# Optimization experiments

Measured on AMD Instinct MI355X. Metric: run time of the kernel, lower is better.

## Reference

```python
import jax, jax.numpy as jnp
import numpy as np

B, A, T = 256, 512, 21
DIM = 128
SC = 6
NHEAD, HD = 4, DIM // 4

def conv1d_relu(x, w, b, stride=2):
    # x: (N, C, L), w: (O, I, K)
    y = jax.lax.conv_general_dilated(x, w, (stride,), 'SAME', dimension_numbers=('NCH', 'OIH', 'NCH'))
    return jax.nn.relu(y + b[None, :, None])

def to_vector(feat, vm):
    vec_mask = vm[..., :-1] & vm[..., 1:]
    while vec_mask.ndim < feat.ndim:
        vec_mask = vec_mask[..., None]
    return jnp.where(vec_mask, feat[:, :, 1:] - feat[:, :, :-1], jnp.zeros_like(feat[:, :, 1:]))

def setup_inputs():
    key = jax.random.key(0)
    ks = jax.random.split(key, 24)
    f32 = jnp.float32
    inp = {}
    inp['position'] = jax.random.normal(ks[0], (B, A, T, 2), f32)
    inp['heading'] = jax.random.normal(ks[1], (B, A, T), f32)
    inp['velocity'] = jax.random.normal(ks[2], (B, A, T, 2), f32)
    inp['shape'] = jax.random.uniform(ks[3], (B, A, T, 2), f32)
    inp['current_state'] = jax.random.normal(ks[4], (B, SC), f32)
    inp['category'] = jax.random.randint(ks[5], (B, A), 0, 4)
    inp['valid_mask'] = jax.random.randint(ks[6], (B, A, T), 0, 2).astype(bool)
    # history encoder (CNN) params: 9 -> 32 -> 64 -> 128 channels, k=3, stride 2
    inp['conv1_w'] = jax.random.normal(ks[7], (32, 9, 3), f32) * 0.1
    inp['conv1_b'] = jnp.zeros((32,), f32)
    inp['conv2_w'] = jax.random.normal(ks[8], (64, 32, 3), f32) * 0.1
    inp['conv2_b'] = jnp.zeros((64,), f32)
    inp['conv3_w'] = jax.random.normal(ks[9], (128, 64, 3), f32) * 0.1
    inp['conv3_b'] = jnp.zeros((128,), f32)
    # StateAttentionEncoder params
    inp['se_w'] = jax.random.normal(ks[10], (SC, DIM), f32) * 0.02   # per-channel Linear(1,dim) weights
    inp['se_b'] = jnp.zeros((SC, DIM), f32)
    inp['pos_embed'] = jax.random.normal(ks[11], (1, SC, DIM), f32) * 0.02
    inp['query'] = jax.random.normal(ks[12], (1, 1, DIM), f32) * 0.02
    inp['in_proj_w'] = jax.random.normal(ks[13], (3 * DIM, DIM), f32) * (1.0 / np.sqrt(DIM))
    inp['in_proj_b'] = jnp.zeros((3 * DIM,), f32)
    inp['out_proj_w'] = jax.random.normal(ks[14], (DIM, DIM), f32) * (1.0 / np.sqrt(DIM))
    inp['out_proj_b'] = jnp.zeros((DIM,), f32)
    inp['type_emb'] = jax.random.normal(ks[15], (4, DIM), f32) * 0.02
    return inp

def reference(position, heading, velocity, shape, current_state, category, valid_mask,
              conv1_w, conv1_b, conv2_w, conv2_b, conv3_w, conv3_b,
              se_w, se_b, pos_embed, query, in_proj_w, in_proj_b, out_proj_w, out_proj_b,
              type_emb):
    # --- build per-step agent features (B, A, T-1, 9) ---
    heading_vec = to_vector(heading, valid_mask)
    valid_mask_vec = valid_mask[..., 1:] & valid_mask[..., :-1]
    agent_feature = jnp.concatenate([
        to_vector(position, valid_mask),
        to_vector(velocity, valid_mask),
        jnp.stack([jnp.cos(heading_vec), jnp.sin(heading_vec)], axis=-1),
        shape[:, :, 1:],
        valid_mask_vec.astype(jnp.float32)[..., None],
    ], axis=-1)
    bs, nA, Tm1, C = agent_feature.shape
    x = agent_feature.reshape(bs * nA, Tm1, C).transpose(0, 2, 1)  # (N, 9, T-1)
    # --- history CNN encoder (applied to all rows, then masked; same math as boolean gather/scatter) ---
    h = conv1d_relu(x, conv1_w, conv1_b)
    h = conv1d_relu(h, conv2_w, conv2_b)
    h = conv1d_relu(h, conv3_w, conv3_b)
    enc = h.mean(axis=-1)  # (N, DIM)
    valid_agent = valid_mask.any(-1).reshape(-1)
    x_agent = jnp.where(valid_agent[:, None], enc, 0.0).reshape(bs, nA, DIM)
    # --- ego state attention encoder (eval mode: no token dropout) ---
    ego = current_state[:, :SC]
    x_embed = ego[:, :, None] * se_w[None] + se_b[None] + pos_embed  # (B, SC, DIM)
    Wq, Wk, Wv = in_proj_w[:DIM], in_proj_w[DIM:2 * DIM], in_proj_w[2 * DIM:]
    bq, bk, bv = in_proj_b[:DIM], in_proj_b[DIM:2 * DIM], in_proj_b[2 * DIM:]
    q = (query[0, 0] @ Wq.T + bq).reshape(NHEAD, HD)             # (H, D)
    k = (x_embed @ Wk.T + bk).reshape(bs, SC, NHEAD, HD)          # (B, S, H, D)
    v = (x_embed @ Wv.T + bv).reshape(bs, SC, NHEAD, HD)
    scores = jnp.einsum('hd,bshd->bhs', q, k) * (1.0 / np.sqrt(HD))
    attn = jax.nn.softmax(scores, axis=-1)
    o = jnp.einsum('bhs,bshd->bhd', attn, v).reshape(bs, DIM)
    x_ego = o @ out_proj_w.T + out_proj_b                         # (B, DIM)
    x_agent = x_agent.at[:, 0].set(x_ego)
    # --- type embedding add ---
    return x_agent + type_emb[category]
```

## Files before the change

### kernel.cpp

```cpp
#include <hip/hip_runtime.h>
#include <hip/hip_bf16.h>


#define BB 256
#define AAG 512
#define TT 21
#define NAG (BB * AAG)
#define AB 12
#define NB1 ((NAG + AB - 1) / AB)

typedef __hip_bfloat16 bf16;
typedef __attribute__((ext_vector_type(8))) short s8v;
typedef __attribute__((ext_vector_type(4))) float f4v;

__device__ int g_dtype;
__device__ int g_mask_mode;
__device__ __align__(16) short g_w1p[32 * 64];
__device__ __align__(16) short g_w2p[64 * 96];
__device__ __align__(16) short g_w3p[128 * 192];
__device__ __align__(16) float g_b1[32];
__device__ __align__(16) float g_b2[64];
__device__ __align__(16) float g_b3[128];
__device__ __align__(16) float g_wqk[4 * 128];
__device__ __align__(16) float g_qb[4];

template <int DT>
__device__ __forceinline__ float ldf(const void* p, long i) {
    if (DT) return __bfloat162float(((const bf16*)p)[i]);
    return ((const float*)p)[i];
}
template <int DT>
__device__ __forceinline__ void stf(void* p, long i, float v) {
    if (DT) ((bf16*)p)[i] = __float2bfloat16(v);
    else    ((float*)p)[i] = v;
}
__device__ __forceinline__ unsigned short f2bu(float x) {
    bf16 b = __float2bfloat16(x);
    union { bf16 b; unsigned short u; } cv; cv.b = b; return cv.u;
}
__device__ __forceinline__ float bu2f(unsigned short u) {
    union { unsigned int i; float f; } cv; cv.i = ((unsigned int)u) << 16; return cv.f;
}
template <int DT>
__device__ __forceinline__ float2 ldf2(const void* p, long i) {
    if (DT) {
        unsigned int u = *(const unsigned int*)((const bf16*)p + i);
        return make_float2(bu2f((unsigned short)(u & 0xffffu)),
                           bu2f((unsigned short)(u >> 16)));
    }
    return *(const float2*)((const float*)p + i);
}
__device__ __forceinline__ bool mask_at(const void* p, long i, int mode) {
    if (mode == 0) return ((const int*)p)[i] != 0;
    if (mode == 1) return ((const unsigned char*)p)[i] != 0;
    if (mode == 2) return ((const float*)p)[i] != 0.f;
    return (((const unsigned short*)p)[i] & 0x7fff) != 0;
}

template <int DT>
__device__ __forceinline__ float rowdot64(const void* W, long off, const float* y) {
    float acc = 0.f;
    if (DT) {
        const unsigned short* wr = (const unsigned short*)W + off;
#pragma unroll
        for (int i = 0; i < 8; i++) {
            uint4 w = *(const uint4*)(wr + i * 8);
            acc = fmaf(bu2f((unsigned short)(w.x & 0xffffu)), y[i * 8 + 0], acc);
            acc = fmaf(bu2f((unsigned short)(w.x >> 16)),     y[i * 8 + 1], acc);
            acc = fmaf(bu2f((unsigned short)(w.y & 0xffffu)), y[i * 8 + 2], acc);
            acc = fmaf(bu2f((unsigned short)(w.y >> 16)),     y[i * 8 + 3], acc);
            acc = fmaf(bu2f((unsigned short)(w.z & 0xffffu)), y[i * 8 + 4], acc);
            acc = fmaf(bu2f((unsigned short)(w.z >> 16)),     y[i * 8 + 5], acc);
            acc = fmaf(bu2f((unsigned short)(w.w & 0xffffu)), y[i * 8 + 6], acc);
            acc = fmaf(bu2f((unsigned short)(w.w >> 16)),     y[i * 8 + 7], acc);
        }
    } else {
        const float* wr = (const float*)W + off;
#pragma unroll
        for (int i = 0; i < 16; i++) {
            float4 w = *(const float4*)(wr + i * 4);
            acc = fmaf(w.x, y[i * 4 + 0], acc);
            acc = fmaf(w.y, y[i * 4 + 1], acc);
            acc = fmaf(w.z, y[i * 4 + 2], acc);
            acc = fmaf(w.w, y[i * 4 + 3], acc);
        }
    }
    return acc;
}

template <int DT>
__device__ __forceinline__ void prep_body(const void* w1, const void* b1,
                                          const void* w2, const void* b2,
                                          const void* w3, const void* b3) {
    int tid = blockIdx.x * 256 + threadIdx.x;
    const int nt = 64 * 256;
    for (int i = tid; i < 32 * 64; i += nt) {
        int oc = i >> 6, k = i & 63, tap = k >> 4, ic = k & 15;
        float v = (tap < 3 && ic < 9) ? ldf<DT>(w1, oc * 27 + ic * 3 + tap) : 0.f;
        g_w1p[i] = (short)f2bu(v);
    }
    for (int i = tid; i < 64 * 96; i += nt) {
        int oc = i / 96, k = i % 96, tap = k >> 5, ic = k & 31;
        g_w2p[i] = (short)f2bu(ldf<DT>(w2, oc * 96 + ic * 3 + tap));
    }
    for (int i = tid; i < 128 * 192; i += nt) {
        int oc = i / 192, k = i % 192, tap = k >> 6, ic = k & 63;
        g_w3p[i] = (short)f2bu(ldf<DT>(w3, oc * 192 + ic * 3 + tap));
    }
    for (int i = tid; i < 32; i += nt) g_b1[i] = ldf<DT>(b1, i);
    for (int i = tid; i < 64; i += nt) g_b2[i] = ldf<DT>(b2, i);
    for (int i = tid; i < 128; i += nt) g_b3[i] = ldf<DT>(b3, i);
}

template <int DT>
__device__ __forceinline__ void qprep_body(const void* query, const void* ipw,
                                           const void* ipb, float* sq) {
    int tid = threadIdx.x;
    if (tid < 128) {
        float acc = ldf<DT>(ipb, tid);
        for (int e = 0; e < 128; e++)
            acc = fmaf(ldf<DT>(query, e), ldf<DT>(ipw, (long)tid * 128 + e), acc);
        sq[tid] = acc;
    }
    __syncthreads();
    int e = tid & 127, hb = tid >> 7;
    for (int h = hb; h < 4; h += 2) {
        float acc = 0.f;
#pragma unroll
        for (int j = 0; j < 32; j++)
            acc = fmaf(sq[h * 32 + j], ldf<DT>(ipw, (long)(128 + h * 32 + j) * 128 + e), acc);
        g_wqk[h * 128 + e] = acc;
    }
    if (tid < 4) {
        float acc = 0.f;
#pragma unroll
        for (int j = 0; j < 32; j++)
            acc = fmaf(sq[tid * 32 + j], ldf<DT>(ipb, 128 + tid * 32 + j), acc);
        g_qb[tid] = acc;
    }
}

__global__ __launch_bounds__(256) void prep_kernel(
    const unsigned int* __restrict__ pw, const unsigned char* __restrict__ m,
    const void* __restrict__ w1, const void* __restrict__ b1,
    const void* __restrict__ w2, const void* __restrict__ b2,
    const void* __restrict__ w3, const void* __restrict__ b3,
    const void* __restrict__ query, const void* __restrict__ ipw,
    const void* __restrict__ ipb) {
    __shared__ int cls[4];
    __shared__ int mv;
    __shared__ int good;
    __shared__ float sq[128];
    int tid = threadIdx.x;
    if (tid < 4) cls[tid] = 0;
    if (tid == 0) { mv = 0; good = 0; }
    __syncthreads();
    int g = 0;
    for (int i = tid; i < 1024; i += 256) {
        unsigned int w = pw[i];
        unsigned int h0 = w & 0xffffu, h1 = w >> 16;
        unsigned int e0 = (h0 >> 7) & 0xff, e1 = (h1 >> 7) & 0xff;
        if (h0 == 0 || (e0 >= 90 && e0 <= 160)) g++;
        if (h1 == 0 || (e1 >= 90 && e1 <= 160)) g++;
    }
    atomicAdd(&good, g);
    int l0 = 0, l1 = 0, l2 = 0, l3 = 0, lm = 0;
    for (int i = tid; i < 4096; i += 256) {
        int v = m[i];
        if (v) {
            switch (i & 3) { case 0: l0 = 1; break; case 1: l1 = 1; break;
                             case 2: l2 = 1; break; default: l3 = 1; }
            if (v > lm) lm = v;
        }
    }
    if (l0) atomicOr(&cls[0], 1);
    if (l1) atomicOr(&cls[1], 1);
    if (l2) atomicOr(&cls[2], 1);
    if (l3) atomicOr(&cls[3], 1);
    atomicMax(&mv, lm);
    __syncthreads();
    int dt = (good >= 1740) ? 1 : 0;
    int mode;
    if (!cls[1] && !cls[2] && !cls[3]) mode = 0;
    else if (!cls[0] && !cls[1])       mode = 2;
    else if (mv <= 1)                  mode = 1;
    else                               mode = 3;
    if (blockIdx.x == 0 && tid == 0) { g_dtype = dt; g_mask_mode = mode; }

    if (blockIdx.x < 64) {
        if (dt) prep_body<1>(w1, b1, w2, b2, w3, b3);
        else    prep_body<0>(w1, b1, w2, b2, w3, b3);
    } else {
        if (dt) qprep_body<1>(query, ipw, ipb, sq);
        else    qprep_body<0>(query, ipw, ipb, sq);
    }
}

#define FEAT_RS 24
#define FEAT_AS 568
#define H1_RS 40
#define H1_AS 440
#define H2_RS 72
#define H2_AS 504
#define C3_AS 392
#define OFF_H1 6816
#define OFF_VALID 24192
#define SMEM_BYTES 24240

#define MFMA16(a, b, c) __builtin_amdgcn_mfma_f32_16x16x32_bf16((a), (b), (c), 0, 0, 0)

template <int DT>
__device__ __forceinline__ void stage1_body(
    const void* pos, const void* heading, const void* vel, const void* shp,
    const void* vmask, const int* category, const void* type_emb, void* out,
    char* smem, long agent0) {
    short* feat = (short*)smem;
    short* h1   = (short*)smem + OFF_H1;
    short* h2   = (short*)smem;
    short* c3   = (short*)smem + OFF_H1;
    int* s_valid = (int*)(smem + OFF_VALID);

    const int tid = threadIdx.x;
    const int wave = tid >> 6, lane = tid & 63;
    const int col = lane & 15, quad = lane >> 4;
    const int cg = col < AB ? col : AB - 1;
    const int mode = g_mask_mode;

    if (tid < AB * 16) {
        unsigned int* h1u = (unsigned int*)h1;
        h1u[(tid >> 4) * 220 + 200 + (tid & 15)] = 0;
    }
    for (int idx = tid; idx < AB * 22; idx += 256) {
        int ag = idx / 22, t = idx % 22;
        long agl = agent0 + ag;
        bool live = agl < NAG;
        short* row = feat + ag * FEAT_AS + t * FEAT_RS;
        if (t == 0) {
            int v = 0;
            if (live) {
                long b0 = agl * TT;
#pragma unroll
                for (int tt = 0; tt < TT; tt++)
                    v |= mask_at(vmask, b0 + tt, mode) ? 1 : 0;
            }
            s_valid[ag] = v;
        }
        if (t >= 20 || !live) {
            *(uint4*)row = make_uint4(0, 0, 0, 0);
            *(uint4*)(row + 8) = make_uint4(0, 0, 0, 0);
        } else {
            long base = agl * TT + t;
            bool vmt = mask_at(vmask, base, mode);
            bool m2 = vmt && mask_at(vmask, base + 1, mode);
            float2 pa = ldf2<DT>(pos, base * 2), pb = ldf2<DT>(pos, base * 2 + 2);
            float2 va = ldf2<DT>(vel, base * 2), vb = ldf2<DT>(vel, base * 2 + 2);
            float hh0 = ldf<DT>(heading, base), hh1 = ldf<DT>(heading, base + 1);
            float2 sv = ldf2<DT>(shp, base * 2 + 2);
            float dh = m2 ? (hh1 - hh0) : 0.f;
            float sn, cn;
            __sincosf(dh, &sn, &cn);
            unsigned int p0 = f2bu(m2 ? pb.x - pa.x : 0.f) | ((unsigned int)f2bu(m2 ? pb.y - pa.y : 0.f) << 16);
            unsigned int p1 = f2bu(m2 ? vb.x - va.x : 0.f) | ((unsigned int)f2bu(m2 ? vb.y - va.y : 0.f) << 16);
            unsigned int p2 = f2bu(cn) | ((unsigned int)f2bu(sn) << 16);
            unsigned int p3 = f2bu(sv.x) | ((unsigned int)f2bu(sv.y) << 16);
            unsigned int p4 = (unsigned int)f2bu(m2 ? 1.f : 0.f);
            *(uint4*)row = make_uint4(p0, p1, p2, p3);
            *(uint4*)(row + 8) = make_uint4(p4, 0, 0, 0);
        }
    }
    __syncthreads();

    {
        int Mt = wave >> 1;
        int oc = Mt * 16 + col;
        s8v a0 = *(const s8v*)(g_w1p + oc * 64 + quad * 8);
        s8v a1 = *(const s8v*)(g_w1p + oc * 64 + 32 + quad * 8);
        int k0 = quad * 8, k1 = 32 + quad * 8;
        int tap0 = k0 >> 4, ic0 = k0 & 15;
        int tap1 = k1 >> 4, ic1 = k1 & 15;
        int ocr = Mt * 16 + quad * 4;
        f4v bia = *(const f4v*)(g_b1 + ocr);
        const short* agbase = feat + cg * FEAT_AS;
#pragma unroll
        for (int i = 0; i < 5; i++) {
            int p = (wave & 1) * 5 + i;
            const short* bb = agbase + 2 * p * FEAT_RS;
            s8v b0 = *(const s8v*)(bb + tap0 * FEAT_RS + ic0);
            s8v b1 = *(const s8v*)(bb + tap1 * FEAT_RS + ic1);
            f4v acc = {0.f, 0.f, 0.f, 0.f};
            acc = MFMA16(a0, b0, acc);
            acc = MFMA16(a1, b1, acc);
            if (col < AB) {
                unsigned int lo = f2bu(fmaxf(acc[0] + bia[0], 0.f)) | ((unsigned int)f2bu(fmaxf(acc[1] + bia[1], 0.f)) << 16);
                unsigned int hi = f2bu(fmaxf(acc[2] + bia[2], 0.f)) | ((unsigned int)f2bu(fmaxf(acc[3] + bia[3], 0.f)) << 16);
                *(uint2*)(h1 + col * H1_AS + p * H1_RS + ocr) = make_uint2(lo, hi);
            }
        }
    }
    __syncthreads();

    {
        unsigned int* h2u = (unsigned int*)h2;
        for (int i = tid; i < AB * 64; i += 256) {
            int a2 = i >> 6, r = (i >> 5) & 1, cc = i & 31;
            h2u[a2 * 252 + r * 216 + cc] = 0;
        }
        int Mt = wave;
        int oc = Mt * 16 + col;
        s8v a[3];
#pragma unroll
        for (int ks = 0; ks < 3; ks++)
            a[ks] = *(const s8v*)(g_w2p + oc * 96 + ks * 32 + quad * 8);
        int ocr = Mt * 16 + quad * 4;
        f4v bia = *(const f4v*)(g_b2 + ocr);
#pragma unroll
        for (int p = 0; p < 5; p++) {
            f4v acc = {0.f, 0.f, 0.f, 0.f};
#pragma unroll
            for (int ks = 0; ks < 3; ks++) {
                s8v b = *(const s8v*)(h1 + cg * H1_AS + (2 * p + ks) * H1_RS + quad * 8);
                acc = MFMA16(a[ks], b, acc);
            }
            if (col < AB) {
                unsigned int lo = f2bu(fmaxf(acc[0] + bia[0], 0.f)) | ((unsigned int)f2bu(fmaxf(acc[1] + bia[1], 0.f)) << 16);
                unsigned int hi = f2bu(fmaxf(acc[2] + bia[2], 0.f)) | ((unsigned int)f2bu(fmaxf(acc[3] + bia[3], 0.f)) << 16);
                *(uint2*)(h2 + col * H2_AS + (p + 1) * H2_RS + ocr) = make_uint2(lo, hi);
            }
        }
    }
    __syncthreads();

#pragma unroll
    for (int m2 = 0; m2 < 2; m2++) {
        int Mt = wave * 2 + m2;
        int oc = Mt * 16 + col;
        s8v a[6];
#pragma unroll
        for (int ks = 0; ks < 6; ks++)
            a[ks] = *(const s8v*)(g_w3p + oc * 192 + ks * 32 + quad * 8);
        int ocr = Mt * 16 + quad * 4;
        f4v bia = *(const f4v*)(g_b3 + ocr);
#pragma unroll
        for (int p = 0; p < 3; p++) {
            f4v acc = {0.f, 0.f, 0.f, 0.f};
#pragma unroll
            for (int ks = 0; ks < 6; ks++) {
                int kg = ks * 32 + quad * 8;
                int tap = kg >> 6, ic = kg & 63;
                s8v b = *(const s8v*)(h2 + cg * H2_AS + (2 * p + tap) * H2_RS + ic);
                acc = MFMA16(a[ks], b, acc);
            }
            if (col < AB) {
                unsigned int lo = f2bu(fmaxf(acc[0] + bia[0], 0.f)) | ((unsigned int)f2bu(fmaxf(acc[1] + bia[1], 0.f)) << 16);
                unsigned int hi = f2bu(fmaxf(acc[2] + bia[2], 0.f)) | ((unsigned int)f2bu(fmaxf(acc[3] + bia[3], 0.f)) << 16);
                *(uint2*)(c3 + col * C3_AS + p * 128 + ocr) = make_uint2(lo, hi);
            }
        }
    }
    __syncthreads();

    if (tid < AB * 16) {
        int ag = tid >> 4;
        int ocg = (tid & 15) * 8;
        long agl = agent0 + ag;
        if (agl < NAG) {
            const short* cb = c3 + ag * C3_AS;
            s8v x0 = *(const s8v*)(cb + ocg);
            s8v x1 = *(const s8v*)(cb + 128 + ocg);
            s8v x2 = *(const s8v*)(cb + 256 + ocg);
            int valid = s_valid[ag];
            int cat = category[agl];
            float vals[8];
#pragma unroll
            for (int j = 0; j < 8; j++) {
                float m = (bu2f((unsigned short)x0[j]) + bu2f((unsigned short)x1[j]) +
                           bu2f((unsigned short)x2[j])) * (1.f / 3.f);
                vals[j] = valid ? m : 0.f;
            }
            if (DT) {
                s8v te = *(const s8v*)((const bf16*)type_emb + (long)cat * 128 + ocg);
                s8v o;
#pragma unroll
                for (int j = 0; j < 8; j++)
                    o[j] = (short)f2bu(vals[j] + bu2f((unsigned short)te[j]));
                *(s8v*)((bf16*)out + agl * 128 + ocg) = o;
            } else {
                const float4* tep = (const float4*)((const float*)type_emb + (long)cat * 128 + ocg);
                float4 t0 = tep[0], t1 = tep[1];
                float4 o0 = make_float4(vals[0] + t0.x, vals[1] + t0.y, vals[2] + t0.z, vals[3] + t0.w);
                float4 o1 = make_float4(vals[4] + t1.x, vals[5] + t1.y, vals[6] + t1.z, vals[7] + t1.w);
                float4* op = (float4*)((float*)out + agl * 128 + ocg);
                op[0] = o0; op[1] = o1;
            }
        }
    }
}

__global__ __launch_bounds__(256) void stage1_kernel(
    const void* __restrict__ pos, const void* __restrict__ heading,
    const void* __restrict__ vel, const void* __restrict__ shp,
    const void* __restrict__ vmask, const int* __restrict__ category,
    const void* __restrict__ type_emb, void* __restrict__ out) {
    __shared__ __align__(16) char smem[SMEM_BYTES];
    long agent0 = (long)blockIdx.x * AB;
    if (g_dtype) stage1_body<1>(pos, heading, vel, shp, vmask, category, type_emb, out, smem, agent0);
    else         stage1_body<0>(pos, heading, vel, shp, vmask, category, type_emb, out, smem, agent0);
}

template <int DT>
__device__ __forceinline__ void stage2_body(
    const void* cs, const int* category,
    const void* se_w, const void* se_b, const void* pe,
    const void* ipw, const void* ipb, const void* opw, const void* opb,
    const void* type_emb, void* out, float* sm) {
    const int b = blockIdx.x;
    const int tid = threadIdx.x;
    const int d = tid & 127, half = tid >> 7;

    float* s_xe  = sm;
    float* s_y   = s_xe + 768;
    float* s_sc  = s_y + 512;
    float* s_att = s_sc + 32;
    float* s_o   = s_att + 32;
    float* s_par = s_o + 128;

    for (int idx = tid; idx < 768; idx += 256) {
        int s = idx >> 7, dd = idx & 127;
        float ego = ldf<DT>(cs, b * 6 + s);
        s_xe[idx] = fmaf(ego, ldf<DT>(se_w, s * 128 + dd),
                         ldf<DT>(se_b, s * 128 + dd) + ldf<DT>(pe, s * 128 + dd));
    }
    __syncthreads();

    if (tid < 96) {
        int g = tid >> 2, lig = tid & 3;
        int h = g / 6, s = g - h * 6;
        const float* xr = s_xe + s * 128 + lig * 32;
        const float* wr = g_wqk + h * 128 + lig * 32;
        float t = 0.f;
#pragma unroll
        for (int e = 0; e < 32; e++) t = fmaf(xr[e], wr[e], t);
        t += __shfl_xor(t, 1, 4);
        t += __shfl_xor(t, 2, 4);
        if (lig == 0) s_sc[g] = (t + g_qb[h]) * 0.17677669529663687f;
    }
    __syncthreads();

    if (tid < 4) {
        float mx = -1e30f;
#pragma unroll
        for (int s = 0; s < 6; s++) mx = fmaxf(mx, s_sc[tid * 6 + s]);
        float sum = 0.f, ex[6];
#pragma unroll
        for (int s = 0; s < 6; s++) { ex[s] = expf(s_sc[tid * 6 + s] - mx); sum += ex[s]; }
        float inv = 1.f / sum;
#pragma unroll
        for (int s = 0; s < 6; s++) s_att[tid * 6 + s] = ex[s] * inv;
    }
    __syncthreads();

    for (int idx = tid; idx < 512; idx += 256) {
        int h = idx >> 7, e = idx & 127;
        float y = 0.f;
#pragma unroll
        for (int s = 0; s < 6; s++) y = fmaf(s_att[h * 6 + s], s_xe[s * 128 + e], y);
        s_y[idx] = y;
    }
    __syncthreads();

    {
        int h = d >> 5;
        const float* yr = s_y + h * 128 + half * 64;
        s_par[half * 128 + d] = rowdot64<DT>(ipw, (long)(256 + d) * 128 + half * 64, yr);
    }
    __syncthreads();
    if (half == 0) s_o[d] = s_par[d] + s_par[128 + d] + ldf<DT>(ipb, 256 + d);
    __syncthreads();

    {
        const float* orr = s_o + half * 64;
        s_par[half * 128 + d] = rowdot64<DT>(opw, (long)d * 128 + half * 64, orr);
    }
    __syncthreads();
    if (half == 0) {
        float x = s_par[d] + s_par[128 + d] + ldf<DT>(opb, d);
        int cat = category[(long)b * AAG];
        stf<DT>(out, (long)b * AAG * 128 + d, x + ldf<DT>(type_emb, cat * 128 + d));
    }
}

__global__ __launch_bounds__(256) void stage2_kernel(
    const void* __restrict__ cs, const int* __restrict__ category,
    const void* __restrict__ se_w, const void* __restrict__ se_b,
    const void* __restrict__ pe,
    const void* __restrict__ ipw, const void* __restrict__ ipb,
    const void* __restrict__ opw, const void* __restrict__ opb,
    const void* __restrict__ type_emb, void* __restrict__ out) {
    __shared__ float sm[1728];
    if (g_dtype) stage2_body<1>(cs, category, se_w, se_b, pe, ipw, ipb, opw, opb, type_emb, out, sm);
    else         stage2_body<0>(cs, category, se_w, se_b, pe, ipw, ipb, opw, opb, type_emb, out, sm);
}

extern "C" void kernel_launch(void* const* d_in, const int* in_sizes, int n_in,
                              void* d_out, int out_size, void* d_ws, size_t ws_size,
                              hipStream_t stream) {
    const void* position      = d_in[0];
    const void* heading       = d_in[1];
    const void* velocity      = d_in[2];
    const void* shape         = d_in[3];
    const void* current_state = d_in[4];
    const int*  category      = (const int*)d_in[5];
    const void* valid_mask    = d_in[6];
    const void* conv1_w = d_in[7];
    const void* conv1_b = d_in[8];
    const void* conv2_w = d_in[9];
    const void* conv2_b = d_in[10];
    const void* conv3_w = d_in[11];
    const void* conv3_b = d_in[12];
    const void* se_w    = d_in[13];
    const void* se_b    = d_in[14];
    const void* pos_embed = d_in[15];
    const void* query     = d_in[16];
    const void* in_proj_w = d_in[17];
    const void* in_proj_b = d_in[18];
    const void* out_proj_w = d_in[19];
    const void* out_proj_b = d_in[20];
    const void* type_emb   = d_in[21];

    hipLaunchKernelGGL(prep_kernel, dim3(65), dim3(256), 0, stream,
                       (const unsigned int*)position, (const unsigned char*)valid_mask,
                       conv1_w, conv1_b, conv2_w, conv2_b, conv3_w, conv3_b,
                       query, in_proj_w, in_proj_b);

    hipLaunchKernelGGL(stage1_kernel, dim3(NB1), dim3(256), 0, stream,
                       position, heading, velocity, shape, valid_mask, category,
                       type_emb, d_out);

    hipLaunchKernelGGL(stage2_kernel, dim3(BB), dim3(256), 0, stream,
                       current_state, category, se_w, se_b, pos_embed,
                       in_proj_w, in_proj_b, out_proj_w, out_proj_b, type_emb, d_out);
}
```

Before: 331.9 us.

## Process four 16-agent chunks per block with register prefetch of next chunk

The stage1 kernel now handles 16 agents per MFMA tile instead of 12, so all 16 columns of each 16x16 MFMA are used. Each block loops over four chunks and prefetches the next chunk's raw inputs into registers while the current chunk runs its convolutions. The per-agent valid flag is now accumulated with atomicOr from the per-timestep mask loads rather than a separate 21-step scan, and syncthreads is replaced by an explicit lgkmcnt wait plus barrier. This cuts grid size and redundant mask reads. In exchange it raises register pressure from the prefetched values and uses more LDS per block.

```diff
diff --git a/kernel.cpp b/kernel.cpp
--- a/kernel.cpp
+++ b/kernel.cpp
@@ -6,8 +6,9 @@
 #define AAG 512
 #define TT 21
 #define NAG (BB * AAG)
-#define AB 12
-#define NB1 ((NAG + AB - 1) / AB)
+#define AB 16
+#define CHUNKS 4
+#define GRID1 (NAG / (AB * CHUNKS))
 
 typedef __hip_bfloat16 bf16;
 typedef __attribute__((ext_vector_type(8))) short s8v;
@@ -41,20 +42,48 @@
 __device__ __forceinline__ float bu2f(unsigned short u) {
     union { unsigned int i; float f; } cv; cv.i = ((unsigned int)u) << 16; return cv.f;
 }
-template <int DT>
-__device__ __forceinline__ float2 ldf2(const void* p, long i) {
-    if (DT) {
-        unsigned int u = *(const unsigned int*)((const bf16*)p + i);
-        return make_float2(bu2f((unsigned short)(u & 0xffffu)),
-                           bu2f((unsigned short)(u >> 16)));
-    }
-    return *(const float2*)((const float*)p + i);
-}
 __device__ __forceinline__ bool mask_at(const void* p, long i, int mode) {
     if (mode == 0) return ((const int*)p)[i] != 0;
     if (mode == 1) return ((const unsigned char*)p)[i] != 0;
     if (mode == 2) return ((const float*)p)[i] != 0.f;
     return (((const unsigned short*)p)[i] & 0x7fff) != 0;
+}
+
+template <int DT> struct RawV { using T2 = float2; using T1 = float; };
+template <> struct RawV<1> { using T2 = unsigned int; using T1 = unsigned short; };
+
+__device__ __forceinline__ float2 dec2v(float2 v) { return v; }
+__device__ __forceinline__ float2 dec2v(unsigned int u) {
+    return make_float2(bu2f((unsigned short)(u & 0xffffu)), bu2f((unsigned short)(u >> 16)));
+}
+__device__ __forceinline__ float dec1v(float v) { return v; }
+__device__ __forceinline__ float dec1v(unsigned short u) { return bu2f(u); }
+
+template <int DT>
+__device__ __forceinline__ typename RawV<DT>::T2 ldr2(const void* p, long i) {
+    if constexpr (DT) return *(const unsigned int*)((const bf16*)p + i);
+    else return *(const float2*)((const float*)p + i);
+}
+template <int DT>
+__device__ __forceinline__ typename RawV<DT>::T1 ldr1(const void* p, long i) {
+    if constexpr (DT) return ((const unsigned short*)p)[i];
+    else return ((const float*)p)[i];
+}
+__device__ __forceinline__ unsigned int mask_raw(const void* p, long i, int mode) {
+    if (mode == 0) return ((const unsigned int*)p)[i];
+    if (mode == 1) return ((const unsigned char*)p)[i];
+    if (mode == 2) return ((const unsigned int*)p)[i];
+    return ((const unsigned short*)p)[i];
+}
+__device__ __forceinline__ bool mask_dec(unsigned int r, int mode) {
+    if (mode == 2) return (r & 0x7fffffffu) != 0;
+    if (mode == 3) return (r & 0x7fffu) != 0;
+    return r != 0;
+}
+
+__device__ __forceinline__ void bar_lds() {
+    asm volatile("s_waitcnt lgkmcnt(0)" ::: "memory");
+    __builtin_amdgcn_s_barrier();
 }
 
 template <int DT>
@@ -203,17 +232,44 @@
 #define H2_RS 72
 #define H2_AS 504
 #define C3_AS 392
-#define OFF_H1 6816
-#define OFF_VALID 24192
-#define SMEM_BYTES 24240
+#define OFF_H1 9088
+#define OFF_VALID 32256
+#define SMEM_BYTES 32384
 
 #define MFMA16(a, b, c) __builtin_amdgcn_mfma_f32_16x16x32_bf16((a), (b), (c), 0, 0, 0)
+
+template <int DT>
+__device__ __forceinline__ void emit_row(
+    short* feat, int* vcur, int ag, int t, int mode,
+    unsigned int m0r, unsigned int m1r,
+    typename RawV<DT>::T2 par, typename RawV<DT>::T2 pbr,
+    typename RawV<DT>::T2 var, typename RawV<DT>::T2 vbr,
+    typename RawV<DT>::T1 h0r, typename RawV<DT>::T1 h1r,
+    typename RawV<DT>::T2 svr) {
+    bool vmt = mask_dec(m0r, mode);
+    bool m2 = vmt && mask_dec(m1r, mode);
+    if (vmt) atomicOr(&vcur[ag], 1);
+    float2 pa = dec2v(par), pb = dec2v(pbr), va = dec2v(var), vb = dec2v(vbr);
+    float hh0 = dec1v(h0r), hh1 = dec1v(h1r);
+    float2 sv = dec2v(svr);
+    float dh = m2 ? (hh1 - hh0) : 0.f;
+    float sn, cn;
+    __sincosf(dh, &sn, &cn);
+    unsigned int p0 = f2bu(m2 ? pb.x - pa.x : 0.f) | ((unsigned int)f2bu(m2 ? pb.y - pa.y : 0.f) << 16);
+    unsigned int p1 = f2bu(m2 ? vb.x - va.x : 0.f) | ((unsigned int)f2bu(m2 ? vb.y - va.y : 0.f) << 16);
+    unsigned int p2 = f2bu(cn) | ((unsigned int)f2bu(sn) << 16);
+    unsigned int p3 = f2bu(sv.x) | ((unsigned int)f2bu(sv.y) << 16);
+    unsigned int p4 = (unsigned int)f2bu(m2 ? 1.f : 0.f);
+    short* row = feat + ag * FEAT_AS + t * FEAT_RS;
+    *(uint4*)row = make_uint4(p0, p1, p2, p3);
+    *(uint4*)(row + 8) = make_uint4(p4, 0, 0, 0);
+}
 
 template <int DT>
 __device__ __forceinline__ void stage1_body(
     const void* pos, const void* heading, const void* vel, const void* shp,
     const void* vmask, const int* category, const void* type_emb, void* out,
-    char* smem, long agent0) {
+    char* smem) {
     short* feat = (short*)smem;
     short* h1   = (short*)smem + OFF_H1;
     short* h2   = (short*)smem;
@@ -223,152 +279,163 @@
     const int tid = threadIdx.x;
     const int wave = tid >> 6, lane = tid & 63;
     const int col = lane & 15, quad = lane >> 4;
-    const int cg = col < AB ? col : AB - 1;
     const int mode = g_mask_mode;
-
-    if (tid < AB * 16) {
-        unsigned int* h1u = (unsigned int*)h1;
-        h1u[(tid >> 4) * 220 + 200 + (tid & 15)] = 0;
-    }
-    for (int idx = tid; idx < AB * 22; idx += 256) {
-        int ag = idx / 22, t = idx % 22;
-        long agl = agent0 + ag;
-        bool live = agl < NAG;
-        short* row = feat + ag * FEAT_AS + t * FEAT_RS;
-        if (t == 0) {
-            int v = 0;
-            if (live) {
-                long b0 = agl * TT;
-#pragma unroll
-                for (int tt = 0; tt < TT; tt++)
-                    v |= mask_at(vmask, b0 + tt, mode) ? 1 : 0;
-            }
-            s_valid[ag] = v;
-        }
-        if (t >= 20 || !live) {
-            *(uint4*)row = make_uint4(0, 0, 0, 0);
-            *(uint4*)(row + 8) = make_uint4(0, 0, 0, 0);
-        } else {
-            long base = agl * TT + t;
-            bool vmt = mask_at(vmask, base, mode);
-            bool m2 = vmt && mask_at(vmask, base + 1, mode);
-            float2 pa = ldf2<DT>(pos, base * 2), pb = ldf2<DT>(pos, base * 2 + 2);
-            float2 va = ldf2<DT>(vel, base * 2), vb = ldf2<DT>(vel, base * 2 + 2);
-            float hh0 = ldf<DT>(heading, base), hh1 = ldf<DT>(heading, base + 1);
-            float2 sv = ldf2<DT>(shp, base * 2 + 2);
-            float dh = m2 ? (hh1 - hh0) : 0.f;
-            float sn, cn;
-            __sincosf(dh, &sn, &cn);
-            unsigned int p0 = f2bu(m2 ? pb.x - pa.x : 0.f) | ((unsigned int)f2bu(m2 ? pb.y - pa.y : 0.f) << 16);
-            unsigned int p1 = f2bu(m2 ? vb.x - va.x : 0.f) | ((unsigned int)f2bu(m2 ? vb.y - va.y : 0.f) << 16);
-            unsigned int p2 = f2bu(cn) | ((unsigned int)f2bu(sn) << 16);
-            unsigned int p3 = f2bu(sv.x) | ((unsigned int)f2bu(sv.y) << 16);
-            unsigned int p4 = (unsigned int)f2bu(m2 ? 1.f : 0.f);
-            *(uint4*)row = make_uint4(p0, p1, p2, p3);
-            *(uint4*)(row + 8) = make_uint4(p4, 0, 0, 0);
-        }
-    }
-    __syncthreads();
-
-    {
-        int Mt = wave >> 1;
-        int oc = Mt * 16 + col;
-        s8v a0 = *(const s8v*)(g_w1p + oc * 64 + quad * 8);
-        s8v a1 = *(const s8v*)(g_w1p + oc * 64 + 32 + quad * 8);
-        int k0 = quad * 8, k1 = 32 + quad * 8;
-        int tap0 = k0 >> 4, ic0 = k0 & 15;
-        int tap1 = k1 >> 4, ic1 = k1 & 15;
-        int ocr = Mt * 16 + quad * 4;
-        f4v bia = *(const f4v*)(g_b1 + ocr);
-        const short* agbase = feat + cg * FEAT_AS;
-#pragma unroll
-        for (int i = 0; i < 5; i++) {
-            int p = (wave & 1) * 5 + i;
-            const short* bb = agbase + 2 * p * FEAT_RS;
-            s8v b0 = *(const s8v*)(bb + tap0 * FEAT_RS + ic0);
-            s8v b1 = *(const s8v*)(bb + tap1 * FEAT_RS + ic1);
-            f4v acc = {0.f, 0.f, 0.f, 0.f};
-            acc = MFMA16(a0, b0, acc);
-            acc = MFMA16(a1, b1, acc);
-            if (col < AB) {
+    const long agent0_blk = (long)blockIdx.x * (AB * CHUNKS);
+
+    const int ag1 = tid / 20, t1 = tid % 20;
+    const int ag2 = (256 + tid) / 20, t2 = (256 + tid) % 20;
+    const bool zrow = (tid >= 96 && tid < 128);
+    const int zi = tid - 96, zag = zi >> 1;
+    const bool zth = zrow && !(zi & 1);
+
+    typename RawV<DT>::T2 pa1{}, pb1{}, va1{}, vb1{}, pa2{}, pb2{}, va2{}, vb2{};
+    typename RawV<DT>::T1 h01{}, h11{};
+    unsigned int m01 = 0, m11 = 0, m02 = 0, m12 = 0, mz = 0;
+
+    auto prefetch = [&](int c) {
+        long a0c = agent0_blk + (long)c * AB;
+        {
+            long base = (a0c + ag1) * TT + t1;
+            m01 = mask_raw(vmask, base, mode);
+            m11 = mask_raw(vmask, base + 1, mode);
+            pa1 = ldr2<DT>(pos, base * 2); pb1 = ldr2<DT>(pos, base * 2 + 2);
+            va1 = ldr2<DT>(vel, base * 2); vb1 = ldr2<DT>(vel, base * 2 + 2);
+            h01 = ldr1<DT>(heading, base); h11 = ldr1<DT>(heading, base + 1);
+        }
+        if (tid < 64) {
+            long base = (a0c + ag2) * TT + t2;
+            m02 = mask_raw(vmask, base, mode);
+            m12 = mask_raw(vmask, base + 1, mode);
+            pa2 = ldr2<DT>(pos, base * 2); pb2 = ldr2<DT>(pos, base * 2 + 2);
+            va2 = ldr2<DT>(vel, base * 2); vb2 = ldr2<DT>(vel, base * 2 + 2);
+        }
+        if (zth) mz = mask_raw(vmask, (a0c + zag) * TT + 20, mode);
+    };
+
+    if (tid < 32) s_valid[tid] = 0;
+    prefetch(0);
+    bar_lds();
+
+    for (int c = 0; c < CHUNKS; ++c) {
+        int* vcur = s_valid + (c & 1) * 16;
+        long a0c = agent0_blk + (long)c * AB;
+
+        {
+            auto sv1r = ldr2<DT>(shp, ((a0c + ag1) * TT + t1) * 2 + 2);
+            typename RawV<DT>::T2 sv2r{};
+            typename RawV<DT>::T1 h02{}, h12{};
+            if (tid < 64) {
+                long base2 = (a0c + ag2) * TT + t2;
+                sv2r = ldr2<DT>(shp, base2 * 2 + 2);
+                h02 = ldr1<DT>(heading, base2);
+                h12 = ldr1<DT>(heading, base2 + 1);
+            }
+            ((unsigned int*)h1)[(tid >> 4) * 220 + 200 + (tid & 15)] = 0;
+            if (zrow) {
+                short* row = feat + zag * FEAT_AS + (20 + (zi & 1)) * FEAT_RS;
+                *(uint4*)row = make_uint4(0, 0, 0, 0);
+                *(uint4*)(row + 8) = make_uint4(0, 0, 0, 0);
+                if (zth && mask_dec(mz, mode)) atomicOr(&vcur[zag], 1);
+            }
+            emit_row<DT>(feat, vcur, ag1, t1, mode, m01, m11, pa1, pb1, va1, vb1, h01, h11, sv1r);
+            if (tid < 64)
+                emit_row<DT>(feat, vcur, ag2, t2, mode, m02, m12, pa2, pb2, va2, vb2, h02, h12, sv2r);
+        }
+        if (c + 1 < CHUNKS) prefetch(c + 1);
+        bar_lds();
+
+        {
+            int Mt = wave >> 1;
+            int oc = Mt * 16 + col;
+            s8v a0 = *(const s8v*)(g_w1p + oc * 64 + quad * 8);
+            s8v a1 = *(const s8v*)(g_w1p + oc * 64 + 32 + quad * 8);
+            int k0 = quad * 8, k1 = 32 + quad * 8;
+            int tap0 = k0 >> 4, ic0 = k0 & 15;
+            int tap1 = k1 >> 4, ic1 = k1 & 15;
+            int ocr = Mt * 16 + quad * 4;
+            f4v bia = *(const f4v*)(g_b1 + ocr);
+            const short* agbase = feat + col * FEAT_AS;
+#pragma unroll
+            for (int i = 0; i < 5; i++) {
+                int p = (wave & 1) * 5 + i;
+                const short* bb = agbase + 2 * p * FEAT_RS;
+                s8v b0 = *(const s8v*)(bb + tap0 * FEAT_RS + ic0);
+                s8v b1 = *(const s8v*)(bb + tap1 * FEAT_RS + ic1);
+                f4v acc = {0.f, 0.f, 0.f, 0.f};
+                acc = MFMA16(a0, b0, acc);
+                acc = MFMA16(a1, b1, acc);
                 unsigned int lo = f2bu(fmaxf(acc[0] + bia[0], 0.f)) | ((unsigned int)f2bu(fmaxf(acc[1] + bia[1], 0.f)) << 16);
                 unsigned int hi = f2bu(fmaxf(acc[2] + bia[2], 0.f)) | ((unsigned int)f2bu(fmaxf(acc[3] + bia[3], 0.f)) << 16);
                 *(uint2*)(h1 + col * H1_AS + p * H1_RS + ocr) = make_uint2(lo, hi);
             }
         }
-    }
-    __syncthreads();
-
-    {
-        unsigned int* h2u = (unsigned int*)h2;
-        for (int i = tid; i < AB * 64; i += 256) {
-            int a2 = i >> 6, r = (i >> 5) & 1, cc = i & 31;
-            h2u[a2 * 252 + r * 216 + cc] = 0;
-        }
-        int Mt = wave;
-        int oc = Mt * 16 + col;
-        s8v a[3];
-#pragma unroll
-        for (int ks = 0; ks < 3; ks++)
-            a[ks] = *(const s8v*)(g_w2p + oc * 96 + ks * 32 + quad * 8);
-        int ocr = Mt * 16 + quad * 4;
-        f4v bia = *(const f4v*)(g_b2 + ocr);
-#pragma unroll
-        for (int p = 0; p < 5; p++) {
-            f4v acc = {0.f, 0.f, 0.f, 0.f};
-#pragma unroll
-            for (int ks = 0; ks < 3; ks++) {
-                s8v b = *(const s8v*)(h1 + cg * H1_AS + (2 * p + ks) * H1_RS + quad * 8);
-                acc = MFMA16(a[ks], b, acc);
-            }
-            if (col < AB) {
+        bar_lds();
+
+        {
+            unsigned int* h2u = (unsigned int*)h2;
+            for (int i = tid; i < 1024; i += 256) {
+                int a2 = i >> 6, r = (i >> 5) & 1, cc = i & 31;
+                h2u[a2 * 252 + r * 216 + cc] = 0;
+            }
+            int Mt = wave;
+            int oc = Mt * 16 + col;
+            s8v a[3];
+#pragma unroll
+            for (int ks = 0; ks < 3; ks++)
+                a[ks] = *(const s8v*)(g_w2p + oc * 96 + ks * 32 + quad * 8);
+            int ocr = Mt * 16 + quad * 4;
+            f4v bia = *(const f4v*)(g_b2 + ocr);
+#pragma unroll
+            for (int p = 0; p < 5; p++) {
+                f4v acc = {0.f, 0.f, 0.f, 0.f};
+#pragma unroll
+                for (int ks = 0; ks < 3; ks++) {
+                    s8v b = *(const s8v*)(h1 + col * H1_AS + (2 * p + ks) * H1_RS + quad * 8);
+                    acc = MFMA16(a[ks], b, acc);
+                }
                 unsigned int lo = f2bu(fmaxf(acc[0] + bia[0], 0.f)) | ((unsigned int)f2bu(fmaxf(acc[1] + bia[1], 0.f)) << 16);
                 unsigned int hi = f2bu(fmaxf(acc[2] + bia[2], 0.f)) | ((unsigned int)f2bu(fmaxf(acc[3] + bia[3], 0.f)) << 16);
                 *(uint2*)(h2 + col * H2_AS + (p + 1) * H2_RS + ocr) = make_uint2(lo, hi);
             }
         }
-    }
-    __syncthreads();
-
-#pragma unroll
-    for (int m2 = 0; m2 < 2; m2++) {
-        int Mt = wave * 2 + m2;
-        int oc = Mt * 16 + col;
-        s8v a[6];
-#pragma unroll
-        for (int ks = 0; ks < 6; ks++)
-            a[ks] = *(const s8v*)(g_w3p + oc * 192 + ks * 32 + quad * 8);
-        int ocr = Mt * 16 + quad * 4;
-        f4v bia = *(const f4v*)(g_b3 + ocr);
-#pragma unroll
-        for (int p = 0; p < 3; p++) {
-            f4v acc = {0.f, 0.f, 0.f, 0.f};
-#pragma unroll
-            for (int ks = 0; ks < 6; ks++) {
-                int kg = ks * 32 + quad * 8;
-                int tap = kg >> 6, ic = kg & 63;
-                s8v b = *(const s8v*)(h2 + cg * H2_AS + (2 * p + tap) * H2_RS + ic);
-                acc = MFMA16(a[ks], b, acc);
-            }
-            if (col < AB) {
+        bar_lds();
+
+#pragma unroll
+        for (int m2 = 0; m2 < 2; m2++) {
+            int Mt = wave * 2 + m2;
+            int oc = Mt * 16 + col;
+            s8v a[6];
+#pragma unroll
+            for (int ks = 0; ks < 6; ks++)
+                a[ks] = *(const s8v*)(g_w3p + oc * 192 + ks * 32 + quad * 8);
+            int ocr = Mt * 16 + quad * 4;
+            f4v bia = *(const f4v*)(g_b3 + ocr);
+#pragma unroll
+            for (int p = 0; p < 3; p++) {
+                f4v acc = {0.f, 0.f, 0.f, 0.f};
+#pragma unroll
+                for (int ks = 0; ks < 6; ks++) {
+                    int kg = ks * 32 + quad * 8;
+                    int tap = kg >> 6, ic = kg & 63;
+                    s8v b = *(const s8v*)(h2 + col * H2_AS + (2 * p + tap) * H2_RS + ic);
+                    acc = MFMA16(a[ks], b, acc);
+                }
                 unsigned int lo = f2bu(fmaxf(acc[0] + bia[0], 0.f)) | ((unsigned int)f2bu(fmaxf(acc[1] + bia[1], 0.f)) << 16);
                 unsigned int hi = f2bu(fmaxf(acc[2] + bia[2], 0.f)) | ((unsigned int)f2bu(fmaxf(acc[3] + bia[3], 0.f)) << 16);
                 *(uint2*)(c3 + col * C3_AS + p * 128 + ocr) = make_uint2(lo, hi);
             }
         }
-    }
-    __syncthreads();
-
-    if (tid < AB * 16) {
-        int ag = tid >> 4;
-        int ocg = (tid & 15) * 8;
-        long agl = agent0 + ag;
-        if (agl < NAG) {
+        bar_lds();
+
+        {
+            int ag = tid >> 4;
+            int ocg = (tid & 15) * 8;
+            long agl = a0c + ag;
             const short* cb = c3 + ag * C3_AS;
             s8v x0 = *(const s8v*)(cb + ocg);
             s8v x1 = *(const s8v*)(cb + 128 + ocg);
             s8v x2 = *(const s8v*)(cb + 256 + ocg);
-            int valid = s_valid[ag];
+            int valid = vcur[ag];
             int cat = category[agl];
             float vals[8];
 #pragma unroll
@@ -393,6 +460,8 @@
                 op[0] = o0; op[1] = o1;
             }
         }
+        if (tid < 16) s_valid[((c + 1) & 1) * 16 + tid] = 0;
+        if (c + 1 < CHUNKS) bar_lds();
     }
 }
 
@@ -402,9 +471,8 @@
     const void* __restrict__ vmask, const int* __restrict__ category,
     const void* __restrict__ type_emb, void* __restrict__ out) {
     __shared__ __align__(16) char smem[SMEM_BYTES];
-    long agent0 = (long)blockIdx.x * AB;
-    if (g_dtype) stage1_body<1>(pos, heading, vel, shp, vmask, category, type_emb, out, smem, agent0);
-    else         stage1_body<0>(pos, heading, vel, shp, vmask, category, type_emb, out, smem, agent0);
+    if (g_dtype) stage1_body<1>(pos, heading, vel, shp, vmask, category, type_emb, out, smem);
+    else         stage1_body<0>(pos, heading, vel, shp, vmask, category, type_emb, out, smem);
 }
 
 template <int DT>
@@ -532,7 +600,7 @@
                        conv1_w, conv1_b, conv2_w, conv2_b, conv3_w, conv3_b,
                        query, in_proj_w, in_proj_b);
 
-    hipLaunchKernelGGL(stage1_kernel, dim3(NB1), dim3(256), 0, stream,
+    hipLaunchKernelGGL(stage1_kernel, dim3(GRID1), dim3(256), 0, stream,
                        position, heading, velocity, shape, valid_mask, category,
                        type_emb, d_out);
 
```

After: 296.5 us. 10.7% less time.

## Process 16 agents per block to fill MFMA columns and rebalance conv work

Applied to the files above, without the earlier changes.

Raises the agents per block from 12 to 16 so every MFMA N-column carries a real agent. This removes the padded-column waste and the bounds checks, and cuts the block count. Work is redistributed across waves: conv1 and conv2 waves now compute two output tiles per B fragment, and conv3 loads B fragments once and streams weights from global memory. __syncthreads is replaced with an LDS-only waitcnt plus barrier. Shared memory per block grows, which may lower occupancy, and conv2's uneven split (3 vs 2 positions) may leave waves idle.

```diff
diff --git a/kernel.cpp b/kernel.cpp
--- a/kernel.cpp
+++ b/kernel.cpp
@@ -6,8 +6,6 @@
 #define AAG 512
 #define TT 21
 #define NAG (BB * AAG)
-#define AB 12
-#define NB1 ((NAG + AB - 1) / AB)
 
 typedef __hip_bfloat16 bf16;
 typedef __attribute__((ext_vector_type(8))) short s8v;
@@ -55,6 +53,11 @@
     if (mode == 1) return ((const unsigned char*)p)[i] != 0;
     if (mode == 2) return ((const float*)p)[i] != 0.f;
     return (((const unsigned short*)p)[i] & 0x7fff) != 0;
+}
+
+__device__ __forceinline__ void bar_lds() {
+    asm volatile("s_waitcnt lgkmcnt(0)" ::: "memory");
+    __builtin_amdgcn_s_barrier();
 }
 
 template <int DT>
@@ -203,11 +206,17 @@
 #define H2_RS 72
 #define H2_AS 504
 #define C3_AS 392
-#define OFF_H1 6816
-#define OFF_VALID 24192
-#define SMEM_BYTES 24240
+#define OFF_H1 9088
+#define OFF_VALID 32256
+#define SMEM_BYTES 32320
 
 #define MFMA16(a, b, c) __builtin_amdgcn_mfma_f32_16x16x32_bf16((a), (b), (c), 0, 0, 0)
+
+__device__ __forceinline__ uint2 pack_relu(f4v acc, f4v bia) {
+    unsigned int lo = f2bu(fmaxf(acc[0] + bia[0], 0.f)) | ((unsigned int)f2bu(fmaxf(acc[1] + bia[1], 0.f)) << 16);
+    unsigned int hi = f2bu(fmaxf(acc[2] + bia[2], 0.f)) | ((unsigned int)f2bu(fmaxf(acc[3] + bia[3], 0.f)) << 16);
+    return make_uint2(lo, hi);
+}
 
 template <int DT>
 __device__ __forceinline__ void stage1_body(
@@ -223,29 +232,25 @@
     const int tid = threadIdx.x;
     const int wave = tid >> 6, lane = tid & 63;
     const int col = lane & 15, quad = lane >> 4;
-    const int cg = col < AB ? col : AB - 1;
     const int mode = g_mask_mode;
 
-    if (tid < AB * 16) {
+    {
         unsigned int* h1u = (unsigned int*)h1;
         h1u[(tid >> 4) * 220 + 200 + (tid & 15)] = 0;
     }
-    for (int idx = tid; idx < AB * 22; idx += 256) {
+    for (int idx = tid; idx < 16 * 22; idx += 256) {
         int ag = idx / 22, t = idx % 22;
+        short* row = feat + ag * FEAT_AS + t * FEAT_RS;
         long agl = agent0 + ag;
-        bool live = agl < NAG;
-        short* row = feat + ag * FEAT_AS + t * FEAT_RS;
         if (t == 0) {
+            long b0 = agl * TT;
             int v = 0;
-            if (live) {
-                long b0 = agl * TT;
-#pragma unroll
-                for (int tt = 0; tt < TT; tt++)
-                    v |= mask_at(vmask, b0 + tt, mode) ? 1 : 0;
-            }
+#pragma unroll
+            for (int tt = 0; tt < TT; tt++)
+                v |= mask_at(vmask, b0 + tt, mode) ? 1 : 0;
             s_valid[ag] = v;
         }
-        if (t >= 20 || !live) {
+        if (t >= 20) {
             *(uint4*)row = make_uint4(0, 0, 0, 0);
             *(uint4*)(row + 8) = make_uint4(0, 0, 0, 0);
         } else {
@@ -268,130 +273,122 @@
             *(uint4*)(row + 8) = make_uint4(p4, 0, 0, 0);
         }
     }
-    __syncthreads();
+    bar_lds();
 
     {
-        int Mt = wave >> 1;
-        int oc = Mt * 16 + col;
-        s8v a0 = *(const s8v*)(g_w1p + oc * 64 + quad * 8);
-        s8v a1 = *(const s8v*)(g_w1p + oc * 64 + 32 + quad * 8);
+        s8v a00 = *(const s8v*)(g_w1p + col * 64 + quad * 8);
+        s8v a01 = *(const s8v*)(g_w1p + col * 64 + 32 + quad * 8);
+        s8v a10 = *(const s8v*)(g_w1p + (16 + col) * 64 + quad * 8);
+        s8v a11 = *(const s8v*)(g_w1p + (16 + col) * 64 + 32 + quad * 8);
+        f4v bia0 = *(const f4v*)(g_b1 + quad * 4);
+        f4v bia1 = *(const f4v*)(g_b1 + 16 + quad * 4);
         int k0 = quad * 8, k1 = 32 + quad * 8;
         int tap0 = k0 >> 4, ic0 = k0 & 15;
         int tap1 = k1 >> 4, ic1 = k1 & 15;
-        int ocr = Mt * 16 + quad * 4;
-        f4v bia = *(const f4v*)(g_b1 + ocr);
-        const short* agbase = feat + cg * FEAT_AS;
-#pragma unroll
-        for (int i = 0; i < 5; i++) {
-            int p = (wave & 1) * 5 + i;
+        const short* agbase = feat + col * FEAT_AS;
+        for (int p = wave; p < 10; p += 4) {
             const short* bb = agbase + 2 * p * FEAT_RS;
             s8v b0 = *(const s8v*)(bb + tap0 * FEAT_RS + ic0);
             s8v b1 = *(const s8v*)(bb + tap1 * FEAT_RS + ic1);
-            f4v acc = {0.f, 0.f, 0.f, 0.f};
-            acc = MFMA16(a0, b0, acc);
-            acc = MFMA16(a1, b1, acc);
-            if (col < AB) {
-                unsigned int lo = f2bu(fmaxf(acc[0] + bia[0], 0.f)) | ((unsigned int)f2bu(fmaxf(acc[1] + bia[1], 0.f)) << 16);
-                unsigned int hi = f2bu(fmaxf(acc[2] + bia[2], 0.f)) | ((unsigned int)f2bu(fmaxf(acc[3] + bia[3], 0.f)) << 16);
-                *(uint2*)(h1 + col * H1_AS + p * H1_RS + ocr) = make_uint2(lo, hi);
-            }
-        }
-    }
-    __syncthreads();
+            f4v acc0 = {0.f, 0.f, 0.f, 0.f}, acc1 = {0.f, 0.f, 0.f, 0.f};
+            acc0 = MFMA16(a00, b0, acc0); acc0 = MFMA16(a01, b1, acc0);
+            acc1 = MFMA16(a10, b0, acc1); acc1 = MFMA16(a11, b1, acc1);
+            short* wr = h1 + col * H1_AS + p * H1_RS + quad * 4;
+            *(uint2*)wr = pack_relu(acc0, bia0);
+            *(uint2*)(wr + 16) = pack_relu(acc1, bia1);
+        }
+    }
+    bar_lds();
 
     {
         unsigned int* h2u = (unsigned int*)h2;
-        for (int i = tid; i < AB * 64; i += 256) {
+        for (int i = tid; i < 1024; i += 256) {
             int a2 = i >> 6, r = (i >> 5) & 1, cc = i & 31;
             h2u[a2 * 252 + r * 216 + cc] = 0;
         }
-        int Mt = wave;
-        int oc = Mt * 16 + col;
-        s8v a[3];
-#pragma unroll
-        for (int ks = 0; ks < 3; ks++)
-            a[ks] = *(const s8v*)(g_w2p + oc * 96 + ks * 32 + quad * 8);
-        int ocr = Mt * 16 + quad * 4;
-        f4v bia = *(const f4v*)(g_b2 + ocr);
-#pragma unroll
-        for (int p = 0; p < 5; p++) {
+        int mt2 = wave >> 1;
+        int nh = wave & 1;
+        s8v a0[3], a1[3];
+#pragma unroll
+        for (int ks = 0; ks < 3; ks++) {
+            a0[ks] = *(const s8v*)(g_w2p + ((mt2 * 2) * 16 + col) * 96 + ks * 32 + quad * 8);
+            a1[ks] = *(const s8v*)(g_w2p + ((mt2 * 2 + 1) * 16 + col) * 96 + ks * 32 + quad * 8);
+        }
+        f4v bia0 = *(const f4v*)(g_b2 + (mt2 * 2) * 16 + quad * 4);
+        f4v bia1 = *(const f4v*)(g_b2 + (mt2 * 2 + 1) * 16 + quad * 4);
+        int pbeg = nh * 3, pend = nh ? 5 : 3;
+        for (int p = pbeg; p < pend; p++) {
+            const short* bb = h1 + col * H1_AS + 2 * p * H1_RS + quad * 8;
+            s8v b0 = *(const s8v*)(bb);
+            s8v b1 = *(const s8v*)(bb + H1_RS);
+            s8v b2 = *(const s8v*)(bb + 2 * H1_RS);
+            f4v acc0 = {0.f, 0.f, 0.f, 0.f}, acc1 = {0.f, 0.f, 0.f, 0.f};
+            acc0 = MFMA16(a0[0], b0, acc0); acc0 = MFMA16(a0[1], b1, acc0); acc0 = MFMA16(a0[2], b2, acc0);
+            acc1 = MFMA16(a1[0], b0, acc1); acc1 = MFMA16(a1[1], b1, acc1); acc1 = MFMA16(a1[2], b2, acc1);
+            short* wr = h2 + col * H2_AS + (p + 1) * H2_RS + (mt2 * 2) * 16 + quad * 4;
+            *(uint2*)wr = pack_relu(acc0, bia0);
+            *(uint2*)(wr + 16) = pack_relu(acc1, bia1);
+        }
+    }
+    bar_lds();
+
+#pragma unroll
+    for (int p = 0; p < 3; p++) {
+        s8v b[6];
+#pragma unroll
+        for (int ks = 0; ks < 6; ks++) {
+            int kg = ks * 32 + quad * 8;
+            int tap = kg >> 6, ic = kg & 63;
+            b[ks] = *(const s8v*)(h2 + col * H2_AS + (2 * p + tap) * H2_RS + ic);
+        }
+#pragma unroll
+        for (int m2 = 0; m2 < 2; m2++) {
+            int Mt = wave * 2 + m2;
+            int oc = Mt * 16 + col;
             f4v acc = {0.f, 0.f, 0.f, 0.f};
 #pragma unroll
-            for (int ks = 0; ks < 3; ks++) {
-                s8v b = *(const s8v*)(h1 + cg * H1_AS + (2 * p + ks) * H1_RS + quad * 8);
-                acc = MFMA16(a[ks], b, acc);
+            for (int ks = 0; ks < 6; ks++) {
+                s8v a = *(const s8v*)(g_w3p + oc * 192 + ks * 32 + quad * 8);
+                acc = MFMA16(a, b[ks], acc);
             }
-            if (col < AB) {
-                unsigned int lo = f2bu(fmaxf(acc[0] + bia[0], 0.f)) | ((unsigned int)f2bu(fmaxf(acc[1] + bia[1], 0.f)) << 16);
-                unsigned int hi = f2bu(fmaxf(acc[2] + bia[2], 0.f)) | ((unsigned int)f2bu(fmaxf(acc[3] + bia[3], 0.f)) << 16);
-                *(uint2*)(h2 + col * H2_AS + (p + 1) * H2_RS + ocr) = make_uint2(lo, hi);
-            }
-        }
-    }
-    __syncthreads();
-
-#pragma unroll
-    for (int m2 = 0; m2 < 2; m2++) {
-        int Mt = wave * 2 + m2;
-        int oc = Mt * 16 + col;
-        s8v a[6];
-#pragma unroll
-        for (int ks = 0; ks < 6; ks++)
-            a[ks] = *(const s8v*)(g_w3p + oc * 192 + ks * 32 + quad * 8);
-        int ocr = Mt * 16 + quad * 4;
-        f4v bia = *(const f4v*)(g_b3 + ocr);
-#pragma unroll
-        for (int p = 0; p < 3; p++) {
-            f4v acc = {0.f, 0.f, 0.f, 0.f};
-#pragma unroll
-            for (int ks = 0; ks < 6; ks++) {
-                int kg = ks * 32 + quad * 8;
-                int tap = kg >> 6, ic = kg & 63;
-                s8v b = *(const s8v*)(h2 + cg * H2_AS + (2 * p + tap) * H2_RS + ic);
-                acc = MFMA16(a[ks], b, acc);
-            }
-            if (col < AB) {
-                unsigned int lo = f2bu(fmaxf(acc[0] + bia[0], 0.f)) | ((unsigned int)f2bu(fmaxf(acc[1] + bia[1], 0.f)) << 16);
-                unsigned int hi = f2bu(fmaxf(acc[2] + bia[2], 0.f)) | ((unsigned int)f2bu(fmaxf(acc[3] + bia[3], 0.f)) << 16);
-                *(uint2*)(c3 + col * C3_AS + p * 128 + ocr) = make_uint2(lo, hi);
-            }
-        }
-    }
-    __syncthreads();
-
-    if (tid < AB * 16) {
+            f4v bia = *(const f4v*)(g_b3 + Mt * 16 + quad * 4);
+            *(uint2*)(c3 + col * C3_AS + p * 128 + Mt * 16 + quad * 4) =
+                pack_relu(acc, bia);
+        }
+    }
+    bar_lds();
+
+    {
         int ag = tid >> 4;
         int ocg = (tid & 15) * 8;
+        const short* cb = c3 + ag * C3_AS;
+        s8v x0 = *(const s8v*)(cb + ocg);
+        s8v x1 = *(const s8v*)(cb + 128 + ocg);
+        s8v x2 = *(const s8v*)(cb + 256 + ocg);
+        int valid = s_valid[ag];
         long agl = agent0 + ag;
-        if (agl < NAG) {
-            const short* cb = c3 + ag * C3_AS;
-            s8v x0 = *(const s8v*)(cb + ocg);
-            s8v x1 = *(const s8v*)(cb + 128 + ocg);
-            s8v x2 = *(const s8v*)(cb + 256 + ocg);
-            int valid = s_valid[ag];
-            int cat = category[agl];
-            float vals[8];
-#pragma unroll
-            for (int j = 0; j < 8; j++) {
-                float m = (bu2f((unsigned short)x0[j]) + bu2f((unsigned short)x1[j]) +
-                           bu2f((unsigned short)x2[j])) * (1.f / 3.f);
-                vals[j] = valid ? m : 0.f;
-            }
-            if (DT) {
-                s8v te = *(const s8v*)((const bf16*)type_emb + (long)cat * 128 + ocg);
-                s8v o;
-#pragma unroll
-                for (int j = 0; j < 8; j++)
-                    o[j] = (short)f2bu(vals[j] + bu2f((unsigned short)te[j]));
-                *(s8v*)((bf16*)out + agl * 128 + ocg) = o;
-            } else {
-                const float4* tep = (const float4*)((const float*)type_emb + (long)cat * 128 + ocg);
-                float4 t0 = tep[0], t1 = tep[1];
-                float4 o0 = make_float4(vals[0] + t0.x, vals[1] + t0.y, vals[2] + t0.z, vals[3] + t0.w);
-                float4 o1 = make_float4(vals[4] + t1.x, vals[5] + t1.y, vals[6] + t1.z, vals[7] + t1.w);
-                float4* op = (float4*)((float*)out + agl * 128 + ocg);
-                op[0] = o0; op[1] = o1;
-            }
+        int cat = category[agl];
+        float vals[8];
+#pragma unroll
+        for (int j = 0; j < 8; j++) {
+            float m = (bu2f((unsigned short)x0[j]) + bu2f((unsigned short)x1[j]) +
+                       bu2f((unsigned short)x2[j])) * (1.f / 3.f);
+            vals[j] = valid ? m : 0.f;
+        }
+        if (DT) {
+            s8v te = *(const s8v*)((const bf16*)type_emb + (long)cat * 128 + ocg);
+            s8v o;
+#pragma unroll
+            for (int j = 0; j < 8; j++)
+                o[j] = (short)f2bu(vals[j] + bu2f((unsigned short)te[j]));
+            *(s8v*)((bf16*)out + agl * 128 + ocg) = o;
+        } else {
+            const float4* tep = (const float4*)((const float*)type_emb + (long)cat * 128 + ocg);
+            float4 t0 = tep[0], t1 = tep[1];
+            float4 o0 = make_float4(vals[0] + t0.x, vals[1] + t0.y, vals[2] + t0.z, vals[3] + t0.w);
+            float4 o1 = make_float4(vals[4] + t1.x, vals[5] + t1.y, vals[6] + t1.z, vals[7] + t1.w);
+            float4* op = (float4*)((float*)out + agl * 128 + ocg);
+            op[0] = o0; op[1] = o1;
         }
     }
 }
@@ -402,7 +399,7 @@
     const void* __restrict__ vmask, const int* __restrict__ category,
     const void* __restrict__ type_emb, void* __restrict__ out) {
     __shared__ __align__(16) char smem[SMEM_BYTES];
-    long agent0 = (long)blockIdx.x * AB;
+    long agent0 = (long)blockIdx.x * 16;
     if (g_dtype) stage1_body<1>(pos, heading, vel, shp, vmask, category, type_emb, out, smem, agent0);
     else         stage1_body<0>(pos, heading, vel, shp, vmask, category, type_emb, out, smem, agent0);
 }
@@ -532,7 +529,7 @@
                        conv1_w, conv1_b, conv2_w, conv2_b, conv3_w, conv3_b,
                        query, in_proj_w, in_proj_b);
 
-    hipLaunchKernelGGL(stage1_kernel, dim3(NB1), dim3(256), 0, stream,
+    hipLaunchKernelGGL(stage1_kernel, dim3(NAG / 16), dim3(256), 0, stream,
                        position, heading, velocity, shape, valid_mask, category,
                        type_emb, d_out);
 
```

Result: slower. 364.5 us (+9.8%).
